# Kernel optimization log

Hardware: AMD Instinct MI355X
Metric: run time of the kernel (lower is better)

## Reference

```python
import jax, jax.numpy as jnp
import numpy as np

D_IN_Q = 1024
D_IN_KV = 1024
D_OUT_KQ = 1024
D_OUT_V = 1024
N_Q = 4096
N_KV = 4096


def setup_inputs() -> dict:
    key = jax.random.key(0)
    k1, k2, k3, k4, k5 = jax.random.split(key, 5)
    return {
        "x_1": jax.random.normal(k1, (N_Q, D_IN_Q), dtype=jnp.float32),
        "x_2": jax.random.normal(k2, (N_KV, D_IN_KV), dtype=jnp.float32),
        # torch.rand -> uniform [0,1)
        "W_query": jax.random.uniform(k3, (D_IN_Q, D_OUT_KQ), dtype=jnp.float32),
        "W_key": jax.random.uniform(k4, (D_IN_KV, D_OUT_KQ), dtype=jnp.float32),
        "W_value": jax.random.uniform(k5, (D_IN_KV, D_OUT_V), dtype=jnp.float32),
    }


def reference(x_1, x_2, W_query, W_key, W_value):
    d_out_kq = W_query.shape[-1]
    queries = x_1 @ W_query          # [n_q, d_kq]
    keys = x_2 @ W_key               # [n_kv, d_kq]
    values = x_2 @ W_value           # [n_kv, d_v]
    scores = queries @ keys.T        # [n_q, n_kv]
    attn = jax.nn.softmax(scores / jnp.sqrt(jnp.asarray(d_out_kq, scores.dtype)), axis=-1)
    return attn @ values             # [n_q, d_v]
```

## Files before the change

kernel.cpp:

```cpp
#include <hip/hip_runtime.h>
#include <hip/hip_fp16.h>
#include <stdint.h>

typedef _Float16 half8 __attribute__((ext_vector_type(8)));
typedef _Float16 half4v __attribute__((ext_vector_type(4)));
typedef float floatx4 __attribute__((ext_vector_type(4)));

__device__ inline void gload_lds16(const void* g, void* l) {
    __builtin_amdgcn_global_load_lds(
        (const __attribute__((address_space(1))) uint32_t*)g,
        (__attribute__((address_space(3))) uint32_t*)l, 16, 0, 0);
}

__global__ __launch_bounds__(256) void split_cast_all(
    const float* __restrict__ x1, _Float16* __restrict__ x1cat,
    const float* __restrict__ x2, _Float16* __restrict__ x2cat,
    const float* __restrict__ Wk, _Float16* __restrict__ Wkcat,
    const float* __restrict__ Wq, _Float16* __restrict__ Wqcat,
    int nc, int n1, int n2) {
    int i = (blockIdx.x * 256 + threadIdx.x) * 4;
    const float* src;
    _Float16* out;
    bool astyle;
    if (i < 2 * n1) {
        astyle = (i < n1);
        const int ii = astyle ? i : i - n1;
        src = (astyle ? x1 : x2) + ii;
        out = astyle ? x1cat : x2cat;
        i = ii;
    } else {
        int j = i - 2 * n1;
        if (j >= 2 * n2) return;
        astyle = (j < n2);
        const int ii = astyle ? j : j - n2;
        src = (astyle ? Wk : Wq) + ii;
        out = astyle ? Wkcat : Wqcat;
        i = ii;
    }
    float4 v = *(const float4*)src;
    int r = i / nc, c = i % nc;
    half4v hi, lo;
    hi[0] = (_Float16)v.x; lo[0] = (_Float16)(v.x - (float)hi[0]);
    hi[1] = (_Float16)v.y; lo[1] = (_Float16)(v.y - (float)hi[1]);
    hi[2] = (_Float16)v.z; lo[2] = (_Float16)(v.z - (float)hi[2]);
    hi[3] = (_Float16)v.w; lo[3] = (_Float16)(v.w - (float)hi[3]);
    size_t base = (size_t)r * 3 * nc;
    if (astyle) {
        *(half4v*)(out + base + c) = hi;
        *(half4v*)(out + base + nc + c) = lo;
        *(half4v*)(out + base + 2 * nc + c) = hi;
    } else {
        *(half4v*)(out + base + c) = hi;
        *(half4v*)(out + base + nc + c) = hi;
        *(half4v*)(out + base + 2 * nc + c) = lo;
    }
}

__global__ __launch_bounds__(256) void transpose_split_b(
    const float* __restrict__ in, _Float16* __restrict__ out, int dim) {
    __shared__ float tile[32][33];
    const int tx = threadIdx.x, ty = threadIdx.y;
    const int bx = blockIdx.x * 32, by = blockIdx.y * 32;
#pragma unroll
    for (int i = 0; i < 32; i += 8)
        tile[ty + i][tx] = in[(size_t)(by + ty + i) * dim + bx + tx];
    __syncthreads();
#pragma unroll
    for (int i = 0; i < 32; i += 8) {
        float v = tile[tx][ty + i];
        _Float16 hi = (_Float16)v;
        _Float16 lo = (_Float16)(v - (float)hi);
        size_t o = (size_t)(bx + ty + i) * 3 * dim + by + tx;
        out[o] = hi;
        out[o + dim] = hi;
        out[o + 2 * dim] = lo;
    }
}

template <int OMODE>
__global__ __launch_bounds__(512) void gemm_bt8(
    const _Float16* __restrict__ A, const _Float16* __restrict__ B,
    void* __restrict__ Cout, int M, int N, int K, int lda, int ldb,
    float cscale) {
    __shared__ _Float16 As[128 * 64];
    __shared__ _Float16 Bs[128 * 64];

    const int tid  = threadIdx.x;
    const int lane = tid & 63;
    const int wid  = tid >> 6;
    const int wr   = wid >> 1;
    const int wc   = wid & 1;
    const int row0 = blockIdx.y * 128;
    const int col0 = blockIdx.x * 128;

    floatx4 acc[2][4] = {};

    const int srow   = lane >> 3;
    const int schunk = (lane & 7) ^ srow;
    const char* gA = (const char*)(A + (size_t)(row0 + wid * 8 + srow) * lda) + schunk * 16;
    const char* gB = (const char*)(B + (size_t)(col0 + wid * 8 + srow) * ldb) + schunk * 16;
    char* lA = (char*)As + (wid * 8) * 128;
    char* lB = (char*)Bs + (wid * 8) * 128;

    const int frow   = lane & 15;
    const int rxor   = frow & 7;
    const int kchunk = lane >> 4;

    const int kTiles = K >> 6;
    for (int kt = 0; kt < kTiles; ++kt) {
        const size_t kb = (size_t)(kt << 6) * 2;
#pragma unroll
        for (int r = 0; r < 2; ++r) {
            gload_lds16(gA + (size_t)(r * 64) * lda * 2 + kb, lA + r * 64 * 128);
            gload_lds16(gB + (size_t)(r * 64) * ldb * 2 + kb, lB + r * 64 * 128);
        }
        __syncthreads();
#pragma unroll
        for (int kk = 0; kk < 2; ++kk) {
            half8 af[2], bf[4];
            const int pc = ((kk * 4 + kchunk) ^ rxor) * 16;
#pragma unroll
            for (int mi = 0; mi < 2; ++mi)
                af[mi] = *(const half8*)((const char*)As + (wr * 32 + mi * 16 + frow) * 128 + pc);
#pragma unroll
            for (int ni = 0; ni < 4; ++ni)
                bf[ni] = *(const half8*)((const char*)Bs + (wc * 64 + ni * 16 + frow) * 128 + pc);
#pragma unroll
            for (int mi = 0; mi < 2; ++mi)
#pragma unroll
                for (int ni = 0; ni < 4; ++ni)
                    acc[mi][ni] = __builtin_amdgcn_mfma_f32_16x16x32_f16(
                        af[mi], bf[ni], acc[mi][ni], 0, 0, 0);
        }
        __syncthreads();
    }

    const int orow0 = row0 + wr * 32 + ((lane >> 4) << 2);
    const int ocol0 = col0 + wc * 64 + (lane & 15);
#pragma unroll
    for (int mi = 0; mi < 2; ++mi) {
#pragma unroll
        for (int ni = 0; ni < 4; ++ni) {
#pragma unroll
            for (int j = 0; j < 4; ++j) {
                const int rr = orow0 + mi * 16 + j;
                const int cc = ocol0 + ni * 16;
                const float v = acc[mi][ni][j] * cscale;
                if (OMODE == 1) {
                    ((_Float16*)Cout)[(size_t)cc * M + rr] = (_Float16)v;
                } else if (OMODE == 3) {
                    ((float*)Cout)[(size_t)rr * N + cc] = v;
                } else {
                    _Float16 hi = (_Float16)v;
                    _Float16 lo = (_Float16)(v - (float)hi);
                    _Float16* o = (_Float16*)Cout + (size_t)rr * 3 * N + cc;
                    if (OMODE == 4) { o[0] = hi; o[N] = lo; o[2 * N] = hi; }
                    else            { o[0] = hi; o[N] = hi; o[2 * N] = lo; }
                }
            }
        }
    }
}

#define SB0() __builtin_amdgcn_sched_barrier(0)
#define BAR() __builtin_amdgcn_s_barrier()

#define PH_READS(KK, MH, DO_B)                                                \
    {                                                                         \
        const int pc_ = (((KK) * 4 + kchunk) ^ rxor) * 16;                    \
        if (DO_B) {                                                           \
            _Pragma("unroll")                                                 \
            for (int ni = 0; ni < 4; ++ni)                                    \
                bf[ni] = *(const half8*)(bsB + (wc * 64 + ni * 16 + frow) * 128 + pc_); \
        }                                                                     \
        _Pragma("unroll")                                                     \
        for (int mi = 0; mi < 4; ++mi)                                        \
            af[mi] = *(const half8*)(bsA + (wr * 128 + ((MH) * 4 + mi) * 16 + frow) * 128 + pc_); \
    }

#define PH_MFMA(MH)                                                           \
    __builtin_amdgcn_s_setprio(1);                                            \
    _Pragma("unroll")                                                         \
    for (int mi = 0; mi < 4; ++mi)                                            \
        _Pragma("unroll")                                                     \
        for (int ni = 0; ni < 4; ++ni)                                        \
            acc[(MH) * 4 + mi][ni] = __builtin_amdgcn_mfma_f32_16x16x32_f16(  \
                af[mi], bf[ni], acc[(MH) * 4 + mi][ni], 0, 0, 0);             \
    __builtin_amdgcn_s_setprio(0);

#define STG_A(DST, tt, i)                                                     \
    gload_lds16(gA + (size_t)((i) * 64) * lda + (size_t)(tt) * 64,            \
                (char*)(DST) + (wid * 8 + (i) * 64) * 128);
#define STG_B(DST, tt, i)                                                     \
    gload_lds16(gB + (size_t)((i) * 64) * ldb + (size_t)(tt) * 64,            \
                (char*)(DST) + (wid * 8 + (i) * 64) * 128);

__global__ __launch_bounds__(512, 2) void gemm256_bt_f32(
    const _Float16* __restrict__ A, const _Float16* __restrict__ B,
    float* __restrict__ C, int M, int N, int K, int lda, int ldb,
    float cscale) {
    __shared__ _Float16 As[2][256 * 64];
    __shared__ _Float16 Bs[2][256 * 64];

    const int tid  = threadIdx.x;
    const int lane = tid & 63;
    const int wid  = tid >> 6;
    const int wr   = wid >> 2;
    const int wc   = wid & 3;
    const int row0 = blockIdx.y * 256;
    const int col0 = blockIdx.x * 256;

    floatx4 acc[8][4] = {};

    const int srow   = lane >> 3;
    const int schunk = (lane & 7) ^ srow;
    const _Float16* gA = A + (size_t)(row0 + wid * 8 + srow) * lda + schunk * 8;
    const _Float16* gB = B + (size_t)(col0 + wid * 8 + srow) * ldb + schunk * 8;

    const int frow   = lane & 15;
    const int rxor   = frow & 7;
    const int kchunk = lane >> 4;

    const int NT = K >> 6;

#pragma unroll
    for (int i = 0; i < 4; ++i) { STG_A((char*)As[0], 0, i) STG_B((char*)Bs[0], 0, i) }
#pragma unroll
    for (int i = 0; i < 4; ++i) { STG_A((char*)As[1], 1, i) STG_B((char*)Bs[1], 1, i) }
    asm volatile("s_waitcnt vmcnt(8)" ::: "memory");
    SB0();
    BAR();

    half8 af[4], bf[4];
    for (int t = 0; t < NT; ++t) {
        const int d = t & 1;
        char* curA = (char*)As[0] + d * 32768;
        char* curB = (char*)Bs[0] + d * 32768;
        char* nxtA = (char*)As[0] + (d ^ 1) * 32768;
        const char* bsA = curA;
        const char* bsB = curB;

        PH_READS(0, 0, true)
        if (t >= 1 && t + 1 < NT) { STG_A(nxtA, t + 1, 1) STG_A(nxtA, t + 1, 3) }
        SB0();
        BAR();
        asm volatile("s_waitcnt lgkmcnt(0)" ::: "memory");
        SB0();
        PH_MFMA(0)
        BAR();

        PH_READS(0, 1, false)
        SB0();
        BAR();
        asm volatile("s_waitcnt lgkmcnt(0)" ::: "memory");
        SB0();
        PH_MFMA(1)
        BAR();

        PH_READS(1, 0, true)
        SB0();
        BAR();
        asm volatile("s_waitcnt lgkmcnt(0)" ::: "memory");
        SB0();
        PH_MFMA(0)
        BAR();

        PH_READS(1, 1, false)
        const bool pf = (t + 2 < NT);
        if (pf) {
            STG_B(curB, t + 2, 0) STG_B(curB, t + 2, 1)
            STG_B(curB, t + 2, 2) STG_B(curB, t + 2, 3)
            STG_A(curA, t + 2, 0) STG_A(curA, t + 2, 2)
        }
        SB0();
        BAR();
        asm volatile("s_waitcnt lgkmcnt(0)" ::: "memory");
        SB0();
        if (pf) { asm volatile("s_waitcnt vmcnt(6)" ::: "memory"); }
        else    { asm volatile("s_waitcnt vmcnt(0)" ::: "memory"); }
        SB0();
        PH_MFMA(1)
        BAR();
    }

    const int orow0 = row0 + wr * 128 + ((lane >> 4) << 2);
    const int ocol0 = col0 + wc * 64 + frow;
#pragma unroll
    for (int mi = 0; mi < 8; ++mi) {
#pragma unroll
        for (int ni = 0; ni < 4; ++ni) {
#pragma unroll
            for (int j = 0; j < 4; ++j) {
                const int rr = orow0 + mi * 16 + j;
                const int cc = ocol0 + ni * 16;
                C[(size_t)rr * N + cc] = acc[mi][ni][j] * cscale;
            }
        }
    }
}

__global__ __launch_bounds__(256) void softmax_inplace(
    float* __restrict__ S, int ncols) {
    const int row = blockIdx.x;
    float* srow = S + (size_t)row * ncols;
    const int t = threadIdx.x;

    float x[16];
#pragma unroll
    for (int q = 0; q < 4; ++q) {
        float4 v = *(float4*)(srow + t * 16 + q * 4);
        x[q * 4 + 0] = v.x; x[q * 4 + 1] = v.y;
        x[q * 4 + 2] = v.z; x[q * 4 + 3] = v.w;
    }
    float m = x[0];
#pragma unroll
    for (int j = 1; j < 16; ++j) m = fmaxf(m, x[j]);
#pragma unroll
    for (int off = 32; off; off >>= 1) m = fmaxf(m, __shfl_xor(m, off));
    __shared__ float redm[4];
    if ((t & 63) == 0) redm[t >> 6] = m;
    __syncthreads();
    m = fmaxf(fmaxf(redm[0], redm[1]), fmaxf(redm[2], redm[3]));

    float s = 0.0f;
#pragma unroll
    for (int j = 0; j < 16; ++j) {
        x[j] = __expf(x[j] - m);
        s += x[j];
    }
#pragma unroll
    for (int off = 32; off; off >>= 1) s += __shfl_xor(s, off);
    __shared__ float reds[4];
    if ((t & 63) == 0) reds[t >> 6] = s;
    __syncthreads();
    s = reds[0] + reds[1] + reds[2] + reds[3];
    const float inv = 1.0f / s;

    _Float16* prow = (_Float16*)srow;
    half8 o0, o1;
#pragma unroll
    for (int j = 0; j < 8; ++j) {
        o0[j] = (_Float16)(x[j] * inv);
        o1[j] = (_Float16)(x[8 + j] * inv);
    }
    __syncthreads();
    *(half8*)(prow + t * 16)     = o0;
    *(half8*)(prow + t * 16 + 8) = o1;
}

extern "C" void kernel_launch(void* const* d_in, const int* in_sizes, int n_in,
                              void* d_out, int out_size, void* d_ws, size_t ws_size,
                              hipStream_t stream) {
    const float* x1 = (const float*)d_in[0];
    const float* x2 = (const float*)d_in[1];
    const float* Wq = (const float*)d_in[2];
    const float* Wk = (const float*)d_in[3];
    const float* Wv = (const float*)d_in[4];
    float* out = (float*)d_out;

    const int NQ = 4096, NKV = 4096, D = 1024;

    char* ws = (char*)d_ws;
    float*    S      = (float*)ws;
    _Float16* x1cat  = (_Float16*)(ws);
    _Float16* Wqcat  = (_Float16*)(ws + (24u  << 20));
    _Float16* Wkcat  = (_Float16*)(ws + (30u  << 20));
    _Float16* Mtcat  = (_Float16*)(ws + (36u  << 20));
    _Float16* Wvct   = (_Float16*)(ws + (42u  << 20));
    _Float16* x2cat  = (_Float16*)(ws + (64u  << 20));
    _Float16* Tcat   = (_Float16*)(ws + (88u  << 20));
    _Float16* Vt     = (_Float16*)(ws + (112u << 20));

    const int n1 = NQ * D, n2 = D * D;
    split_cast_all<<<(2 * (n1 + n2) + 1023) / 1024, 256, 0, stream>>>(
        x1, x1cat, x2, x2cat, Wk, Wkcat, Wq, Wqcat, D, n1, n2);
    dim3 tb(32, 8), tg(D / 32, D / 32);
    transpose_split_b<<<tg, tb, 0, stream>>>(Wv, Wvct, D);

    gemm_bt8<5><<<dim3(D / 128, D / 128), 512, 0, stream>>>(
        Wkcat, Wqcat, Mtcat, D, D, 3 * D, 3 * D, 3 * D, 1.0f);

    gemm_bt8<4><<<dim3(D / 128, NQ / 128), 512, 0, stream>>>(
        x1cat, Mtcat, Tcat, NQ, D, 3 * D, 3 * D, 3 * D, 1.0f);

    gemm_bt8<1><<<dim3(D / 128, NKV / 128), 512, 0, stream>>>(
        x2cat, Wvct, Vt, NKV, D, D, 3 * D, 3 * D, 1.0f);

    gemm256_bt_f32<<<dim3(NKV / 256, NQ / 256), 512, 0, stream>>>(
        Tcat, x2cat, S, NQ, NKV, 3 * D, 3 * D, 3 * D, 1.0f / 32.0f);

    softmax_inplace<<<NQ, 256, 0, stream>>>(S, NKV);

    gemm_bt8<3><<<dim3(D / 128, NQ / 128), 512, 0, stream>>>(
        (const _Float16*)S, Vt, out, NQ, D, NKV, 2 * NKV, NKV, 1.0f);
}
```

Baseline: 317.6 us.

## Split B tile into two K-halves to spread prefetch across phases

Splits the B shared-memory tile into two K-half buffers with their own swizzle. The first half's refill is now issued after its last read in phase 1, instead of loading all of B in phase 3. This spreads global-to-LDS traffic more evenly across the four MFMA phases and issues the refill earlier. It changes the vmcnt accounting, which must stay correct: waits still count 6 outstanding loads, but the issue order now differs.

Measured after the change: 316.8 us. Within noise of the previous version (-0.3%).

```diff
diff --git a/kernel.cpp b/kernel.cpp
--- a/kernel.cpp
+++ b/kernel.cpp
@@ -165,17 +165,19 @@
 #define SB0() __builtin_amdgcn_sched_barrier(0)
 #define BAR() __builtin_amdgcn_s_barrier()
 
-#define PH_READS(KK, MH, DO_B)                                                \
+#define RD_A4(KK, MH)                                                         \
     {                                                                         \
         const int pc_ = (((KK) * 4 + kchunk) ^ rxor) * 16;                    \
-        if (DO_B) {                                                           \
-            _Pragma("unroll")                                                 \
-            for (int ni = 0; ni < 4; ++ni)                                    \
-                bf[ni] = *(const half8*)(bsB + (wc * 64 + ni * 16 + frow) * 128 + pc_); \
-        }                                                                     \
         _Pragma("unroll")                                                     \
         for (int mi = 0; mi < 4; ++mi)                                        \
             af[mi] = *(const half8*)(bsA + (wr * 128 + ((MH) * 4 + mi) * 16 + frow) * 128 + pc_); \
+    }
+
+#define RD_B4(BUF)                                                            \
+    {                                                                         \
+        _Pragma("unroll")                                                     \
+        for (int ni = 0; ni < 4; ++ni)                                        \
+            bf[ni] = *(const half8*)((BUF) + (wc * 64 + ni * 16 + frow) * 64 + bco); \
     }
 
 #define PH_MFMA(MH)                                                           \
@@ -191,16 +193,17 @@
 #define STG_A(DST, tt, i)                                                     \
     gload_lds16(gA + (size_t)((i) * 64) * lda + (size_t)(tt) * 64,            \
                 (char*)(DST) + (wid * 8 + (i) * 64) * 128);
-#define STG_B(DST, tt, i)                                                     \
-    gload_lds16(gB + (size_t)((i) * 64) * ldb + (size_t)(tt) * 64,            \
-                (char*)(DST) + (wid * 8 + (i) * 64) * 128);
+#define STG_B2(DST, tt, HALF, i)                                              \
+    gload_lds16(gB2 + (size_t)((i) * 128) * ldb + (size_t)(tt) * 64 + (HALF) * 32, \
+                (char*)(DST) + (wid * 16 + (i) * 128) * 64);
 
 __global__ __launch_bounds__(512, 2) void gemm256_bt_f32(
     const _Float16* __restrict__ A, const _Float16* __restrict__ B,
     float* __restrict__ C, int M, int N, int K, int lda, int ldb,
     float cscale) {
     __shared__ _Float16 As[2][256 * 64];
-    __shared__ _Float16 Bs[2][256 * 64];
+    __shared__ _Float16 Bs0[2][256 * 32];
+    __shared__ _Float16 Bs1[2][256 * 32];
 
     const int tid  = threadIdx.x;
     const int lane = tid & 63;
@@ -215,18 +218,24 @@
     const int srow   = lane >> 3;
     const int schunk = (lane & 7) ^ srow;
     const _Float16* gA = A + (size_t)(row0 + wid * 8 + srow) * lda + schunk * 8;
-    const _Float16* gB = B + (size_t)(col0 + wid * 8 + srow) * ldb + schunk * 8;
+    const _Float16* gB2 = B + (size_t)(col0 + wid * 16 + (lane >> 2)) * ldb
+                            + ((lane & 3) ^ ((lane >> 3) & 3)) * 8;
 
     const int frow   = lane & 15;
     const int rxor   = frow & 7;
     const int kchunk = lane >> 4;
+    const int bco    = (kchunk ^ ((frow >> 1) & 3)) * 16;
 
     const int NT = K >> 6;
 
 #pragma unroll
-    for (int i = 0; i < 4; ++i) { STG_A((char*)As[0], 0, i) STG_B((char*)Bs[0], 0, i) }
-#pragma unroll
-    for (int i = 0; i < 4; ++i) { STG_A((char*)As[1], 1, i) STG_B((char*)Bs[1], 1, i) }
+    for (int i = 0; i < 4; ++i) { STG_A((char*)As[0], 0, i) }
+#pragma unroll
+    for (int i = 0; i < 2; ++i) { STG_B2((char*)Bs0[0], 0, 0, i) STG_B2((char*)Bs1[0], 0, 1, i) }
+#pragma unroll
+    for (int i = 0; i < 4; ++i) { STG_A((char*)As[1], 1, i) }
+#pragma unroll
+    for (int i = 0; i < 2; ++i) { STG_B2((char*)Bs0[1], 1, 0, i) STG_B2((char*)Bs1[1], 1, 1, i) }
     asm volatile("s_waitcnt vmcnt(8)" ::: "memory");
     SB0();
     BAR();
@@ -234,13 +243,15 @@
     half8 af[4], bf[4];
     for (int t = 0; t < NT; ++t) {
         const int d = t & 1;
-        char* curA = (char*)As[0] + d * 32768;
-        char* curB = (char*)Bs[0] + d * 32768;
-        char* nxtA = (char*)As[0] + (d ^ 1) * 32768;
+        char* curA  = (char*)As[0]  + d * 32768;
+        char* nxtA  = (char*)As[0]  + (d ^ 1) * 32768;
+        char* curB0 = (char*)Bs0[0] + d * 16384;
+        char* curB1 = (char*)Bs1[0] + d * 16384;
         const char* bsA = curA;
-        const char* bsB = curB;
-
-        PH_READS(0, 0, true)
+        const bool pf = (t + 2 < NT);
+
+        RD_A4(0, 0)
+        RD_B4(curB0)
         if (t >= 1 && t + 1 < NT) { STG_A(nxtA, t + 1, 1) STG_A(nxtA, t + 1, 3) }
         SB0();
         BAR();
@@ -249,7 +260,8 @@
         PH_MFMA(0)
         BAR();
 
-        PH_READS(0, 1, false)
+        RD_A4(0, 1)
+        if (pf) { STG_B2(curB0, t + 2, 0, 0) STG_B2(curB0, t + 2, 0, 1) }
         SB0();
         BAR();
         asm volatile("s_waitcnt lgkmcnt(0)" ::: "memory");
@@ -257,7 +269,8 @@
         PH_MFMA(1)
         BAR();
 
-        PH_READS(1, 0, true)
+        RD_A4(1, 0)
+        RD_B4(curB1)
         SB0();
         BAR();
         asm volatile("s_waitcnt lgkmcnt(0)" ::: "memory");
@@ -265,11 +278,9 @@
         PH_MFMA(0)
         BAR();
 
-        PH_READS(1, 1, false)
-        const bool pf = (t + 2 < NT);
+        RD_A4(1, 1)
         if (pf) {
-            STG_B(curB, t + 2, 0) STG_B(curB, t + 2, 1)
-            STG_B(curB, t + 2, 2) STG_B(curB, t + 2, 3)
+            STG_B2(curB1, t + 2, 1, 0) STG_B2(curB1, t + 2, 1, 1)
             STG_A(curA, t + 2, 0) STG_A(curA, t + 2, 2)
         }
         SB0();
```
